# Kernel tuning notes

Hardware: AMD Instinct MI355X
Metric: run time of the kernel (lower is better)

Reference implementation:

```python
import math
import jax, jax.numpy as jnp
import numpy as np

B, W, C = 2, 2048, 1024
N, K = 16, 64  # heads, head dim (C // N)


def setup_inputs() -> dict:
    key = jax.random.key(0)
    ks = jax.random.split(key, 6)
    return {
        "in_sequence_bwc": jax.random.normal(ks[0], (B, W, C), dtype=jnp.float32),
        "W_proj": jax.random.normal(ks[1], (C, C), dtype=jnp.float32) * (1.0 / math.sqrt(C)),
        "b_proj": jax.random.normal(ks[2], (C,), dtype=jnp.float32) * 0.01,
        "generators_1nwk": jax.random.normal(ks[3], (1, N, W, K), dtype=jnp.float32),
        "W_mix": jax.random.normal(ks[4], (C, C), dtype=jnp.float32) * (1.0 / math.sqrt(C)),
        "b_mix": jax.random.normal(ks[5], (C,), dtype=jnp.float32) * 0.01,
    }


def reference(in_sequence_bwc, W_proj, b_proj, generators_1nwk, W_mix, b_mix):
    b, w, c = in_sequence_bwc.shape
    # shared projection (torch Linear: x @ W.T + b)
    p_bwc = in_sequence_bwc @ W_proj.T + b_proj
    p_bnwk = p_bwc.reshape(b, w, N, K).transpose(0, 2, 1, 3)  # [b, n, w, k]
    g_nwk = generators_1nwk[0, :, :w, :]  # [n, w, k]
    # data-dependent metric generator: p^T @ G -> [b, n, k, k]
    m_bnkk = jnp.einsum("bnwk,nwl->bnkl", p_bnwk, g_nwk)
    tril_kk = jnp.tril(jnp.ones((K, K), dtype=in_sequence_bwc.dtype))
    m_bnkk = m_bnkk * tril_kk  # lower-triangular mask on k x k
    m_bnkk = m_bnkk @ jnp.swapaxes(m_bnkk, -1, -2)  # PSD metric M M^T
    # bilinear scores: P @ M @ P^T, scaled
    pm_bnwk = jnp.einsum("bnwk,bnkl->bnwl", p_bnwk, m_bnkk)
    scores_bnww = jnp.einsum("bnwk,bnvk->bnwv", pm_bnwk, p_bnwk) / math.sqrt(K)
    causal = jnp.tril(jnp.ones((w, w), dtype=bool))
    scores_bnww = jnp.where(causal, scores_bnww, -jnp.inf)
    attn_bnww = jax.nn.softmax(scores_bnww, axis=-1)
    nudged_bnwk = attn_bnww @ p_bnwk
    nudged_bwc = nudged_bnwk.transpose(0, 2, 1, 3).reshape(b, w, c)
    return nudged_bwc @ W_mix.T + b_mix
```

## Files before the change

### kernel.cpp

```cpp
#include <hip/hip_runtime.h>
#include <math.h>

#define B_  2
#define W_  2048
#define C_  1024
#define NH_ 16
#define KD_ 64

__device__ __forceinline__ int sw(int r, int c) {
    return (r << 6) + ((((c >> 2) ^ ((r >> 2) & 7)) << 2) | (c & 3));
}

__device__ __forceinline__ void stage64s(const float* __restrict__ src,
                                         float* dst, int tid) {
#pragma unroll
    for (int q = 0; q < 4; ++q) {
        int idx = tid + (q << 8);
        int r   = idx >> 4;
        int c   = (idx & 15) << 2;
        *(float4*)&dst[sw(r, c)] = *(const float4*)(src + (idx << 2));
    }
}

__device__ __forceinline__ void stage64(const float* __restrict__ src,
                                        float (*dst)[68], int tid) {
#pragma unroll
    for (int q = 0; q < 4; ++q) {
        int idx = tid + (q << 8);
        int e   = idx << 2;
        int r   = e >> 6;
        int c   = e & 63;
        *(float4*)&dst[r][c] = *(const float4*)(src + e);
    }
}

template<int OUT_P_LAYOUT>
__global__ __launch_bounds__(256, 2)
void gemm_nt(const float* __restrict__ A, const float* __restrict__ Bw,
             const float* __restrict__ bias, float* __restrict__ Cout)
{
    __shared__ float As[16][68];
    __shared__ float Bs[16][68];
    const int tid = threadIdx.x;
    const int tx  = tid & 15, ty = tid >> 4;
    const int m0  = blockIdx.x << 6;
    const int n0  = blockIdx.y << 6;
    const int lrow = tid >> 2;
    const int lkq  = (tid & 3) << 2;
    const float* Ap = A  + (size_t)(m0 + lrow) * C_ + lkq;
    const float* Bp = Bw + (size_t)(n0 + lrow) * C_ + lkq;

    float acc[4][4] = {};
    for (int k0 = 0; k0 < C_; k0 += 16) {
        float4 av = *(const float4*)(Ap + k0);
        float4 bv = *(const float4*)(Bp + k0);
        __syncthreads();
        As[lkq+0][lrow] = av.x; As[lkq+1][lrow] = av.y;
        As[lkq+2][lrow] = av.z; As[lkq+3][lrow] = av.w;
        Bs[lkq+0][lrow] = bv.x; Bs[lkq+1][lrow] = bv.y;
        Bs[lkq+2][lrow] = bv.z; Bs[lkq+3][lrow] = bv.w;
        __syncthreads();
#pragma unroll
        for (int kk = 0; kk < 16; ++kk) {
            float4 a4 = *(const float4*)&As[kk][ty << 2];
            float4 b4 = *(const float4*)&Bs[kk][tx << 2];
            float am[4] = {a4.x, a4.y, a4.z, a4.w};
            float bm[4] = {b4.x, b4.y, b4.z, b4.w};
#pragma unroll
            for (int i = 0; i < 4; ++i)
#pragma unroll
                for (int j = 0; j < 4; ++j)
                    acc[i][j] = fmaf(am[i], bm[j], acc[i][j]);
        }
    }

    const int gc = n0 + (tx << 2);
    float4 bb = *(const float4*)&bias[gc];
#pragma unroll
    for (int i = 0; i < 4; ++i) {
        int gm = m0 + (ty << 2) + i;
        float4 o;
        o.x = acc[i][0] + bb.x;
        o.y = acc[i][1] + bb.y;
        o.z = acc[i][2] + bb.z;
        o.w = acc[i][3] + bb.w;
        if (OUT_P_LAYOUT) {
            int b = gm >> 11;
            int w = gm & 2047;
            int n = gc >> 6;
            int k = gc & 63;
            *(float4*)(Cout + (((size_t)(b * NH_ + n) * W_ + w) * KD_ + k)) = o;
        } else {
            *(float4*)(Cout + (size_t)gm * C_ + gc) = o;
        }
    }
}

__global__ __launch_bounds__(256, 2)
void metric_part(const float* __restrict__ p, const float* __restrict__ g,
                 float* __restrict__ part)
{
    __shared__ float Ps[32][68];
    __shared__ float Gs[32][68];
    const int ch  = blockIdx.x;
    const int bn  = blockIdx.y;
    const int n   = bn & (NH_ - 1);
    const int tid = threadIdx.x;
    const int tx  = tid & 15, ty = tid >> 4;
    const float* pb = p + (size_t)bn * W_ * KD_ + (size_t)(ch << 8) * KD_;
    const float* gb = g + (size_t)n  * W_ * KD_ + (size_t)(ch << 8) * KD_;

    float acc[4][4] = {};
    for (int w0 = 0; w0 < 256; w0 += 32) {
        __syncthreads();
#pragma unroll
        for (int q = 0; q < 2; ++q) {
            int idx = tid + (q << 8);
            int e   = idx << 2;
            int r   = e >> 6;
            int c   = e & 63;
            *(float4*)&Ps[r][c] = *(const float4*)(pb + (size_t)(w0 + r) * KD_ + c);
            *(float4*)&Gs[r][c] = *(const float4*)(gb + (size_t)(w0 + r) * KD_ + c);
        }
        __syncthreads();
#pragma unroll 8
        for (int w = 0; w < 32; ++w) {
            float4 a4 = *(const float4*)&Ps[w][ty << 2];
            float4 b4 = *(const float4*)&Gs[w][tx << 2];
            float am[4] = {a4.x, a4.y, a4.z, a4.w};
            float bm[4] = {b4.x, b4.y, b4.z, b4.w};
#pragma unroll
            for (int i = 0; i < 4; ++i)
#pragma unroll
                for (int j = 0; j < 4; ++j)
                    acc[i][j] = fmaf(am[i], bm[j], acc[i][j]);
        }
    }

    float* ob = part + (size_t)(bn * 8 + ch) * KD_ * KD_;
#pragma unroll
    for (int i = 0; i < 4; ++i) {
        float4 o; o.x = acc[i][0]; o.y = acc[i][1]; o.z = acc[i][2]; o.w = acc[i][3];
        *(float4*)(ob + ((ty << 2) + i) * KD_ + (tx << 2)) = o;
    }
}

__global__ __launch_bounds__(256, 2)
void metric_reduce(const float* __restrict__ part, float* __restrict__ m2)
{
    __shared__ float M1s[64][68];
    const int bn  = blockIdx.x;
    const int tid = threadIdx.x;
    const int tx  = tid & 15, ty = tid >> 4;
    const float* pb = part + (size_t)bn * 8 * KD_ * KD_;

#pragma unroll
    for (int v = 0; v < 4; ++v) {
        int f = tid + (v << 8);
        int e = f << 2;
        float4 s = *(const float4*)(pb + e);
#pragma unroll
        for (int c = 1; c < 8; ++c) {
            float4 t = *(const float4*)(pb + c * 4096 + e);
            s.x += t.x; s.y += t.y; s.z += t.z; s.w += t.w;
        }
        int k = e >> 6, l = e & 63;
        if (l + 0 > k) s.x = 0.f;
        if (l + 1 > k) s.y = 0.f;
        if (l + 2 > k) s.z = 0.f;
        if (l + 3 > k) s.w = 0.f;
        *(float4*)&M1s[k][l] = s;
    }
    __syncthreads();

    float a2[4][4] = {};
#pragma unroll
    for (int jq = 0; jq < 64; jq += 4) {
        float4 av[4], bv[4];
#pragma unroll
        for (int i = 0; i < 4; ++i) av[i] = *(const float4*)&M1s[(ty << 2) + i][jq];
#pragma unroll
        for (int j = 0; j < 4; ++j) bv[j] = *(const float4*)&M1s[(tx << 2) + j][jq];
#pragma unroll
        for (int i = 0; i < 4; ++i)
#pragma unroll
            for (int j = 0; j < 4; ++j)
                a2[i][j] += av[i].x * bv[j].x + av[i].y * bv[j].y +
                            av[i].z * bv[j].z + av[i].w * bv[j].w;
    }

    float* ob = m2 + (size_t)bn * KD_ * KD_;
#pragma unroll
    for (int i = 0; i < 4; ++i) {
        float4 o; o.x = a2[i][0]; o.y = a2[i][1]; o.z = a2[i][2]; o.w = a2[i][3];
        *(float4*)(ob + ((ty << 2) + i) * KD_ + (tx << 2)) = o;
    }
}

__global__ __launch_bounds__(256, 2)
void qgen_k(const float* __restrict__ p, const float* __restrict__ m2,
            float* __restrict__ qout)
{
    __shared__ float Pt[64][68];
    __shared__ float Ms[64][68];
    const int bn  = blockIdx.y;
    const int w0  = blockIdx.x << 6;
    const int tid = threadIdx.x;
    const int tx  = tid & 15, ty = tid >> 4;
    const float* pb = p  + (size_t)bn * W_ * KD_ + (size_t)w0 * KD_;
    const float* mb = m2 + (size_t)bn * KD_ * KD_;

    stage64(pb, Pt, tid);
    stage64(mb, Ms, tid);
    __syncthreads();

    float acc[4][4] = {};
#pragma unroll
    for (int kq = 0; kq < 64; kq += 4) {
        float4 av[4];
        float  bm[4][4];
#pragma unroll
        for (int i = 0; i < 4; ++i) av[i] = *(const float4*)&Pt[(ty << 2) + i][kq];
#pragma unroll
        for (int kk = 0; kk < 4; ++kk) {
            float4 t = *(const float4*)&Ms[kq + kk][tx << 2];
            bm[kk][0] = t.x; bm[kk][1] = t.y; bm[kk][2] = t.z; bm[kk][3] = t.w;
        }
#pragma unroll
        for (int i = 0; i < 4; ++i) {
            float am[4] = {av[i].x, av[i].y, av[i].z, av[i].w};
#pragma unroll
            for (int j = 0; j < 4; ++j)
                acc[i][j] = fmaf(am[0], bm[0][j],
                            fmaf(am[1], bm[1][j],
                            fmaf(am[2], bm[2][j],
                            fmaf(am[3], bm[3][j], acc[i][j]))));
        }
    }

    float* ob = qout + (size_t)bn * W_ * KD_ + (size_t)w0 * KD_;
#pragma unroll
    for (int i = 0; i < 4; ++i) {
        float4 o;
        o.x = acc[i][0] * 0.125f; o.y = acc[i][1] * 0.125f;
        o.z = acc[i][2] * 0.125f; o.w = acc[i][3] * 0.125f;
        *(float4*)(ob + ((ty << 2) + i) * KD_ + (tx << 2)) = o;
    }
}

__global__ __launch_bounds__(256, 2)
void attn_k(const float* __restrict__ qg, const float* __restrict__ p,
            float* __restrict__ nud)
{
    __shared__ float Qs[4096];
    __shared__ float Ks[4096];
    __shared__ float Es[4096];
    const int bid = blockIdx.x;
    const int bn  = bid & 31;
    const int qt  = 31 - (bid >> 5);
    const int b   = bn >> 4, n = bn & 15;
    const int tid = threadIdx.x;
    const int tx  = tid & 15, ty = tid >> 4;
    const float* qb = qg + (size_t)bn * W_ * KD_ + (size_t)(qt << 6) * KD_;
    const float* kb = p  + (size_t)bn * W_ * KD_;

    stage64s(qb, Qs, tid);

    float acc[4][4] = {};
    float mi[4], li[4];
#pragma unroll
    for (int i = 0; i < 4; ++i) { mi[i] = -INFINITY; li[i] = 0.f; }

    for (int j0 = 0; j0 <= qt; ++j0) {
        __syncthreads();
        stage64s(kb + (size_t)(j0 << 6) * KD_, Ks, tid);
        __syncthreads();

        float s[4][4] = {};
#pragma unroll
        for (int kq = 0; kq < 64; kq += 4) {
            float4 av[4], bv[4];
#pragma unroll
            for (int i = 0; i < 4; ++i) av[i] = *(const float4*)&Qs[sw((ty << 2) + i, kq)];
#pragma unroll
            for (int j = 0; j < 4; ++j) bv[j] = *(const float4*)&Ks[sw((tx << 2) + j, kq)];
#pragma unroll
            for (int i = 0; i < 4; ++i)
#pragma unroll
                for (int j = 0; j < 4; ++j)
                    s[i][j] = fmaf(av[i].x, bv[j].x,
                              fmaf(av[i].y, bv[j].y,
                              fmaf(av[i].z, bv[j].z,
                              fmaf(av[i].w, bv[j].w, s[i][j]))));
        }

        if (j0 == qt) {
#pragma unroll
            for (int i = 0; i < 4; ++i)
#pragma unroll
                for (int j = 0; j < 4; ++j)
                    if (((tx << 2) + j) > ((ty << 2) + i)) s[i][j] = -INFINITY;
        }

        float mnew[4], al[4];
#pragma unroll
        for (int i = 0; i < 4; ++i) {
            float rm = fmaxf(fmaxf(s[i][0], s[i][1]), fmaxf(s[i][2], s[i][3]));
            rm = fmaxf(rm, __shfl_xor(rm, 1, 16));
            rm = fmaxf(rm, __shfl_xor(rm, 2, 16));
            rm = fmaxf(rm, __shfl_xor(rm, 4, 16));
            rm = fmaxf(rm, __shfl_xor(rm, 8, 16));
            mnew[i] = fmaxf(mi[i], rm);
        }
#pragma unroll
        for (int i = 0; i < 4; ++i) {
#pragma unroll
            for (int j = 0; j < 4; ++j) s[i][j] = __expf(s[i][j] - mnew[i]);
            float rs = s[i][0] + s[i][1] + s[i][2] + s[i][3];
            rs += __shfl_xor(rs, 1, 16);
            rs += __shfl_xor(rs, 2, 16);
            rs += __shfl_xor(rs, 4, 16);
            rs += __shfl_xor(rs, 8, 16);
            al[i] = __expf(mi[i] - mnew[i]);
            li[i] = li[i] * al[i] + rs;
            mi[i] = mnew[i];
        }
#pragma unroll
        for (int i = 0; i < 4; ++i) {
            float4 e; e.x = s[i][0]; e.y = s[i][1]; e.z = s[i][2]; e.w = s[i][3];
            *(float4*)&Es[sw((ty << 2) + i, tx << 2)] = e;
#pragma unroll
            for (int j = 0; j < 4; ++j) acc[i][j] *= al[i];
        }
        __syncthreads();

#pragma unroll
        for (int jq = 0; jq < 64; jq += 4) {
            float4 av[4];
            float  vm[4][4];
#pragma unroll
            for (int i = 0; i < 4; ++i) av[i] = *(const float4*)&Es[sw((ty << 2) + i, jq)];
#pragma unroll
            for (int kk = 0; kk < 4; ++kk) {
                float4 t = *(const float4*)&Ks[sw(jq + kk, tx << 2)];
                vm[kk][0] = t.x; vm[kk][1] = t.y; vm[kk][2] = t.z; vm[kk][3] = t.w;
            }
#pragma unroll
            for (int i = 0; i < 4; ++i) {
                float am[4] = {av[i].x, av[i].y, av[i].z, av[i].w};
#pragma unroll
                for (int c = 0; c < 4; ++c)
                    acc[i][c] = fmaf(am[0], vm[0][c],
                                fmaf(am[1], vm[1][c],
                                fmaf(am[2], vm[2][c],
                                fmaf(am[3], vm[3][c], acc[i][c]))));
            }
        }
    }

    const int wrow = qt << 6;
#pragma unroll
    for (int i = 0; i < 4; ++i) {
        float inv = 1.f / li[i];
        float4 o;
        o.x = acc[i][0] * inv; o.y = acc[i][1] * inv;
        o.z = acc[i][2] * inv; o.w = acc[i][3] * inv;
        size_t row = (size_t)(b * W_ + wrow + (ty << 2) + i);
        *(float4*)(nud + row * C_ + (n << 6) + (tx << 2)) = o;
    }
}

extern "C" void kernel_launch(void* const* d_in, const int* in_sizes, int n_in,
                              void* d_out, int out_size, void* d_ws, size_t ws_size,
                              hipStream_t stream)
{
    (void)in_sizes; (void)n_in; (void)out_size; (void)ws_size;
    const float* X  = (const float*)d_in[0];
    const float* Wp = (const float*)d_in[1];
    const float* bp = (const float*)d_in[2];
    const float* G  = (const float*)d_in[3];
    const float* Wm = (const float*)d_in[4];
    const float* bm = (const float*)d_in[5];
    float* out = (float*)d_out;
    float* ws  = (float*)d_ws;

    float* Pbuf = ws;
    float* Qbuf = ws + 4194304;
    float* M2   = ws + 8388608;
    float* Nud  = ws + 8519680;
    float* Part = Qbuf;

    dim3 blk(256);
    gemm_nt<1>   <<<dim3(64, 16), blk, 0, stream>>>(X, Wp, bp, Pbuf);
    metric_part  <<<dim3(8, 32),  blk, 0, stream>>>(Pbuf, G, Part);
    metric_reduce<<<dim3(32),     blk, 0, stream>>>(Part, M2);
    qgen_k       <<<dim3(32, 32), blk, 0, stream>>>(Pbuf, M2, Qbuf);
    attn_k       <<<dim3(1024),   blk, 0, stream>>>(Qbuf, Pbuf, Nud);
    gemm_nt<0>   <<<dim3(64, 16), blk, 0, stream>>>(Nud, Wm, bm, out);
}
```

Baseline: 842.6 us.

## Use 128x128 register-prefetched GEMMs and fuse Q generation into 128-row attention

```diff
diff --git a/kernel.cpp b/kernel.cpp
--- a/kernel.cpp
+++ b/kernel.cpp
@@ -7,91 +7,104 @@
 #define NH_ 16
 #define KD_ 64
 
-__device__ __forceinline__ int sw(int r, int c) {
+__device__ __forceinline__ int swz2(int r, int c) {
     return (r << 6) + ((((c >> 2) ^ ((r >> 2) & 7)) << 2) | (c & 3));
 }
-
-__device__ __forceinline__ void stage64s(const float* __restrict__ src,
-                                         float* dst, int tid) {
-#pragma unroll
-    for (int q = 0; q < 4; ++q) {
-        int idx = tid + (q << 8);
-        int r   = idx >> 4;
-        int c   = (idx & 15) << 2;
-        *(float4*)&dst[sw(r, c)] = *(const float4*)(src + (idx << 2));
-    }
-}
-
-__device__ __forceinline__ void stage64(const float* __restrict__ src,
-                                        float (*dst)[68], int tid) {
-#pragma unroll
-    for (int q = 0; q < 4; ++q) {
-        int idx = tid + (q << 8);
-        int e   = idx << 2;
-        int r   = e >> 6;
-        int c   = e & 63;
-        *(float4*)&dst[r][c] = *(const float4*)(src + e);
+__device__ __forceinline__ int swz3(int r, int c) {
+    return (r << 6) + ((((c >> 2) ^ ((r >> 3) & 7)) << 2) | (c & 3));
+}
+
+__device__ __forceinline__ void stage_sw2(const float* __restrict__ src,
+                                          float* dst, int tid, int nf4) {
+    for (int idx = tid; idx < nf4; idx += 256) {
+        int r = idx >> 4;
+        int c = (idx & 15) << 2;
+        *(float4*)&dst[swz2(r, c)] = *(const float4*)(src + (idx << 2));
     }
 }
 
 template<int OUT_P_LAYOUT>
 __global__ __launch_bounds__(256, 2)
-void gemm_nt(const float* __restrict__ A, const float* __restrict__ Bw,
+void gemm128(const float* __restrict__ A, const float* __restrict__ Bw,
              const float* __restrict__ bias, float* __restrict__ Cout)
 {
-    __shared__ float As[16][68];
-    __shared__ float Bs[16][68];
+    __shared__ float As[8192];
+    __shared__ float Bs[8192];
     const int tid = threadIdx.x;
     const int tx  = tid & 15, ty = tid >> 4;
-    const int m0  = blockIdx.x << 6;
-    const int n0  = blockIdx.y << 6;
-    const int lrow = tid >> 2;
-    const int lkq  = (tid & 3) << 2;
-    const float* Ap = A  + (size_t)(m0 + lrow) * C_ + lkq;
-    const float* Bp = Bw + (size_t)(n0 + lrow) * C_ + lkq;
-
-    float acc[4][4] = {};
-    for (int k0 = 0; k0 < C_; k0 += 16) {
-        float4 av = *(const float4*)(Ap + k0);
-        float4 bv = *(const float4*)(Bp + k0);
-        __syncthreads();
-        As[lkq+0][lrow] = av.x; As[lkq+1][lrow] = av.y;
-        As[lkq+2][lrow] = av.z; As[lkq+3][lrow] = av.w;
-        Bs[lkq+0][lrow] = bv.x; Bs[lkq+1][lrow] = bv.y;
-        Bs[lkq+2][lrow] = bv.z; Bs[lkq+3][lrow] = bv.w;
-        __syncthreads();
-#pragma unroll
-        for (int kk = 0; kk < 16; ++kk) {
-            float4 a4 = *(const float4*)&As[kk][ty << 2];
-            float4 b4 = *(const float4*)&Bs[kk][tx << 2];
-            float am[4] = {a4.x, a4.y, a4.z, a4.w};
-            float bm[4] = {b4.x, b4.y, b4.z, b4.w};
-#pragma unroll
-            for (int i = 0; i < 4; ++i)
-#pragma unroll
-                for (int j = 0; j < 4; ++j)
-                    acc[i][j] = fmaf(am[i], bm[j], acc[i][j]);
-        }
-    }
-
-    const int gc = n0 + (tx << 2);
-    float4 bb = *(const float4*)&bias[gc];
-#pragma unroll
-    for (int i = 0; i < 4; ++i) {
-        int gm = m0 + (ty << 2) + i;
-        float4 o;
-        o.x = acc[i][0] + bb.x;
-        o.y = acc[i][1] + bb.y;
-        o.z = acc[i][2] + bb.z;
-        o.w = acc[i][3] + bb.w;
-        if (OUT_P_LAYOUT) {
-            int b = gm >> 11;
-            int w = gm & 2047;
-            int n = gc >> 6;
-            int k = gc & 63;
-            *(float4*)(Cout + (((size_t)(b * NH_ + n) * W_ + w) * KD_ + k)) = o;
-        } else {
-            *(float4*)(Cout + (size_t)gm * C_ + gc) = o;
+    const int m0  = blockIdx.x << 7;
+    const int n0  = blockIdx.y << 7;
+
+    float4 ra[8], rb[8];
+    int rr[8], cc[8];
+#pragma unroll
+    for (int t = 0; t < 8; ++t) {
+        int idx = tid + (t << 8);
+        rr[t] = idx >> 4;
+        cc[t] = (idx & 15) << 2;
+    }
+#pragma unroll
+    for (int t = 0; t < 8; ++t) {
+        ra[t] = *(const float4*)(A  + (size_t)(m0 + rr[t]) * C_ + cc[t]);
+        rb[t] = *(const float4*)(Bw + (size_t)(n0 + rr[t]) * C_ + cc[t]);
+    }
+
+    float acc[8][8] = {};
+    for (int kb = 0; kb < 16; ++kb) {
+        __syncthreads();
+#pragma unroll
+        for (int t = 0; t < 8; ++t) {
+            *(float4*)&As[swz3(rr[t], cc[t])] = ra[t];
+            *(float4*)&Bs[swz3(rr[t], cc[t])] = rb[t];
+        }
+        __syncthreads();
+        if (kb < 15) {
+            int k0 = (kb + 1) << 6;
+#pragma unroll
+            for (int t = 0; t < 8; ++t) {
+                ra[t] = *(const float4*)(A  + (size_t)(m0 + rr[t]) * C_ + k0 + cc[t]);
+                rb[t] = *(const float4*)(Bw + (size_t)(n0 + rr[t]) * C_ + k0 + cc[t]);
+            }
+        }
+#pragma unroll
+        for (int kq = 0; kq < 64; kq += 4) {
+            float4 av[8], bv[8];
+#pragma unroll
+            for (int i = 0; i < 8; ++i) av[i] = *(const float4*)&As[swz3((ty << 3) + i, kq)];
+#pragma unroll
+            for (int j = 0; j < 8; ++j) bv[j] = *(const float4*)&Bs[swz3((tx << 3) + j, kq)];
+#pragma unroll
+            for (int i = 0; i < 8; ++i)
+#pragma unroll
+                for (int j = 0; j < 8; ++j)
+                    acc[i][j] = fmaf(av[i].x, bv[j].x,
+                                fmaf(av[i].y, bv[j].y,
+                                fmaf(av[i].z, bv[j].z,
+                                fmaf(av[i].w, bv[j].w, acc[i][j]))));
+        }
+    }
+
+#pragma unroll
+    for (int h = 0; h < 2; ++h) {
+        int gc = n0 + (tx << 3) + (h << 2);
+        float4 bb = *(const float4*)&bias[gc];
+#pragma unroll
+        for (int i = 0; i < 8; ++i) {
+            int gm = m0 + (ty << 3) + i;
+            float4 o;
+            o.x = acc[i][(h << 2) + 0] + bb.x;
+            o.y = acc[i][(h << 2) + 1] + bb.y;
+            o.z = acc[i][(h << 2) + 2] + bb.z;
+            o.w = acc[i][(h << 2) + 3] + bb.w;
+            if (OUT_P_LAYOUT) {
+                int b = gm >> 11;
+                int w = gm & 2047;
+                int n = gc >> 6;
+                int k = gc & 63;
+                *(float4*)(Cout + (((size_t)(b * NH_ + n) * W_ + w) * KD_ + k)) = o;
+            } else {
+                *(float4*)(Cout + (size_t)gm * C_ + gc) = o;
+            }
         }
     }
 }
@@ -198,174 +211,143 @@
 }
 
 __global__ __launch_bounds__(256, 2)
-void qgen_k(const float* __restrict__ p, const float* __restrict__ m2,
-            float* __restrict__ qout)
-{
-    __shared__ float Pt[64][68];
-    __shared__ float Ms[64][68];
-    const int bn  = blockIdx.y;
-    const int w0  = blockIdx.x << 6;
-    const int tid = threadIdx.x;
-    const int tx  = tid & 15, ty = tid >> 4;
-    const float* pb = p  + (size_t)bn * W_ * KD_ + (size_t)w0 * KD_;
-    const float* mb = m2 + (size_t)bn * KD_ * KD_;
-
-    stage64(pb, Pt, tid);
-    stage64(mb, Ms, tid);
-    __syncthreads();
-
-    float acc[4][4] = {};
-#pragma unroll
-    for (int kq = 0; kq < 64; kq += 4) {
-        float4 av[4];
-        float  bm[4][4];
-#pragma unroll
-        for (int i = 0; i < 4; ++i) av[i] = *(const float4*)&Pt[(ty << 2) + i][kq];
-#pragma unroll
-        for (int kk = 0; kk < 4; ++kk) {
-            float4 t = *(const float4*)&Ms[kq + kk][tx << 2];
-            bm[kk][0] = t.x; bm[kk][1] = t.y; bm[kk][2] = t.z; bm[kk][3] = t.w;
-        }
-#pragma unroll
-        for (int i = 0; i < 4; ++i) {
-            float am[4] = {av[i].x, av[i].y, av[i].z, av[i].w};
-#pragma unroll
-            for (int j = 0; j < 4; ++j)
-                acc[i][j] = fmaf(am[0], bm[0][j],
-                            fmaf(am[1], bm[1][j],
-                            fmaf(am[2], bm[2][j],
-                            fmaf(am[3], bm[3][j], acc[i][j]))));
-        }
-    }
-
-    float* ob = qout + (size_t)bn * W_ * KD_ + (size_t)w0 * KD_;
-#pragma unroll
-    for (int i = 0; i < 4; ++i) {
-        float4 o;
-        o.x = acc[i][0] * 0.125f; o.y = acc[i][1] * 0.125f;
-        o.z = acc[i][2] * 0.125f; o.w = acc[i][3] * 0.125f;
-        *(float4*)(ob + ((ty << 2) + i) * KD_ + (tx << 2)) = o;
-    }
-}
-
-__global__ __launch_bounds__(256, 2)
-void attn_k(const float* __restrict__ qg, const float* __restrict__ p,
-            float* __restrict__ nud)
-{
-    __shared__ float Qs[4096];
+void attn_k2(const float* __restrict__ p, const float* __restrict__ m2,
+             float* __restrict__ nud)
+{
+    __shared__ float Qs[8192];
     __shared__ float Ks[4096];
-    __shared__ float Es[4096];
+    __shared__ float Es[8192];
     const int bid = blockIdx.x;
     const int bn  = bid & 31;
-    const int qt  = 31 - (bid >> 5);
+    const int qt  = 15 - (bid >> 5);
     const int b   = bn >> 4, n = bn & 15;
     const int tid = threadIdx.x;
     const int tx  = tid & 15, ty = tid >> 4;
-    const float* qb = qg + (size_t)bn * W_ * KD_ + (size_t)(qt << 6) * KD_;
-    const float* kb = p  + (size_t)bn * W_ * KD_;
-
-    stage64s(qb, Qs, tid);
-
-    float acc[4][4] = {};
-    float mi[4], li[4];
-#pragma unroll
-    for (int i = 0; i < 4; ++i) { mi[i] = -INFINITY; li[i] = 0.f; }
-
-    for (int j0 = 0; j0 <= qt; ++j0) {
-        __syncthreads();
-        stage64s(kb + (size_t)(j0 << 6) * KD_, Ks, tid);
-        __syncthreads();
-
-        float s[4][4] = {};
+    const float* pb = p + (size_t)bn * W_ * KD_;
+    const float* qb = pb + (size_t)(qt << 7) * KD_;
+
+    stage_sw2(qb, Es, tid, 2048);
+    stage_sw2(m2 + (size_t)bn * KD_ * KD_, Ks, tid, 1024);
+    __syncthreads();
+    {
+        float qacc[8][4] = {};
 #pragma unroll
         for (int kq = 0; kq < 64; kq += 4) {
-            float4 av[4], bv[4];
-#pragma unroll
-            for (int i = 0; i < 4; ++i) av[i] = *(const float4*)&Qs[sw((ty << 2) + i, kq)];
-#pragma unroll
-            for (int j = 0; j < 4; ++j) bv[j] = *(const float4*)&Ks[sw((tx << 2) + j, kq)];
-#pragma unroll
-            for (int i = 0; i < 4; ++i)
+            float4 av[8], bm[4];
+#pragma unroll
+            for (int i = 0; i < 8; ++i) av[i] = *(const float4*)&Es[swz2((ty << 3) + i, kq)];
+#pragma unroll
+            for (int kk = 0; kk < 4; ++kk) bm[kk] = *(const float4*)&Ks[swz2(kq + kk, tx << 2)];
+#pragma unroll
+            for (int i = 0; i < 8; ++i) {
+                qacc[i][0] = fmaf(av[i].x, bm[0].x, fmaf(av[i].y, bm[1].x,
+                             fmaf(av[i].z, bm[2].x, fmaf(av[i].w, bm[3].x, qacc[i][0]))));
+                qacc[i][1] = fmaf(av[i].x, bm[0].y, fmaf(av[i].y, bm[1].y,
+                             fmaf(av[i].z, bm[2].y, fmaf(av[i].w, bm[3].y, qacc[i][1]))));
+                qacc[i][2] = fmaf(av[i].x, bm[0].z, fmaf(av[i].y, bm[1].z,
+                             fmaf(av[i].z, bm[2].z, fmaf(av[i].w, bm[3].z, qacc[i][2]))));
+                qacc[i][3] = fmaf(av[i].x, bm[0].w, fmaf(av[i].y, bm[1].w,
+                             fmaf(av[i].z, bm[2].w, fmaf(av[i].w, bm[3].w, qacc[i][3]))));
+            }
+        }
+#pragma unroll
+        for (int i = 0; i < 8; ++i) {
+            float4 o;
+            o.x = qacc[i][0] * 0.125f; o.y = qacc[i][1] * 0.125f;
+            o.z = qacc[i][2] * 0.125f; o.w = qacc[i][3] * 0.125f;
+            *(float4*)&Qs[swz2((ty << 3) + i, tx << 2)] = o;
+        }
+    }
+
+    float acc[8][4] = {};
+    float mi[8], li[8];
+#pragma unroll
+    for (int i = 0; i < 8; ++i) { mi[i] = -INFINITY; li[i] = 0.f; }
+
+    const int j0max = (qt << 1) + 1;
+    for (int j0 = 0; j0 <= j0max; ++j0) {
+        __syncthreads();
+        stage_sw2(pb + (size_t)(j0 << 6) * KD_, Ks, tid, 1024);
+        __syncthreads();
+
+        float s[8][4] = {};
+#pragma unroll
+        for (int kq = 0; kq < 64; kq += 4) {
+            float4 bv[4];
+#pragma unroll
+            for (int j = 0; j < 4; ++j) bv[j] = *(const float4*)&Ks[swz2((tx << 2) + j, kq)];
+#pragma unroll
+            for (int i = 0; i < 8; ++i) {
+                float4 a = *(const float4*)&Qs[swz2((ty << 3) + i, kq)];
 #pragma unroll
                 for (int j = 0; j < 4; ++j)
-                    s[i][j] = fmaf(av[i].x, bv[j].x,
-                              fmaf(av[i].y, bv[j].y,
-                              fmaf(av[i].z, bv[j].z,
-                              fmaf(av[i].w, bv[j].w, s[i][j]))));
-        }
-
-        if (j0 == qt) {
-#pragma unroll
-            for (int i = 0; i < 4; ++i)
+                    s[i][j] = fmaf(a.x, bv[j].x, fmaf(a.y, bv[j].y,
+                              fmaf(a.z, bv[j].z, fmaf(a.w, bv[j].w, s[i][j]))));
+            }
+        }
+
+        if (j0 >= (qt << 1)) {
+            int cbase = (j0 << 6) - (qt << 7) + (tx << 2);
+#pragma unroll
+            for (int i = 0; i < 8; ++i)
 #pragma unroll
                 for (int j = 0; j < 4; ++j)
-                    if (((tx << 2) + j) > ((ty << 2) + i)) s[i][j] = -INFINITY;
-        }
-
-        float mnew[4], al[4];
-#pragma unroll
-        for (int i = 0; i < 4; ++i) {
+                    if (cbase + j > (ty << 3) + i) s[i][j] = -INFINITY;
+        }
+
+#pragma unroll
+        for (int i = 0; i < 8; ++i) {
             float rm = fmaxf(fmaxf(s[i][0], s[i][1]), fmaxf(s[i][2], s[i][3]));
             rm = fmaxf(rm, __shfl_xor(rm, 1, 16));
             rm = fmaxf(rm, __shfl_xor(rm, 2, 16));
             rm = fmaxf(rm, __shfl_xor(rm, 4, 16));
             rm = fmaxf(rm, __shfl_xor(rm, 8, 16));
-            mnew[i] = fmaxf(mi[i], rm);
-        }
-#pragma unroll
-        for (int i = 0; i < 4; ++i) {
-#pragma unroll
-            for (int j = 0; j < 4; ++j) s[i][j] = __expf(s[i][j] - mnew[i]);
+            float mnew = fmaxf(mi[i], rm);
+#pragma unroll
+            for (int j = 0; j < 4; ++j) s[i][j] = __expf(s[i][j] - mnew);
             float rs = s[i][0] + s[i][1] + s[i][2] + s[i][3];
             rs += __shfl_xor(rs, 1, 16);
             rs += __shfl_xor(rs, 2, 16);
             rs += __shfl_xor(rs, 4, 16);
             rs += __shfl_xor(rs, 8, 16);
-            al[i] = __expf(mi[i] - mnew[i]);
-            li[i] = li[i] * al[i] + rs;
-            mi[i] = mnew[i];
-        }
-#pragma unroll
-        for (int i = 0; i < 4; ++i) {
+            float al = __expf(mi[i] - mnew);
+            li[i] = li[i] * al + rs;
+            mi[i] = mnew;
             float4 e; e.x = s[i][0]; e.y = s[i][1]; e.z = s[i][2]; e.w = s[i][3];
-            *(float4*)&Es[sw((ty << 2) + i, tx << 2)] = e;
-#pragma unroll
-            for (int j = 0; j < 4; ++j) acc[i][j] *= al[i];
+            *(float4*)&Es[swz2((ty << 3) + i, tx << 2)] = e;
+#pragma unroll
+            for (int j = 0; j < 4; ++j) acc[i][j] *= al;
         }
         __syncthreads();
 
 #pragma unroll
         for (int jq = 0; jq < 64; jq += 4) {
-            float4 av[4];
-            float  vm[4][4];
-#pragma unroll
-            for (int i = 0; i < 4; ++i) av[i] = *(const float4*)&Es[sw((ty << 2) + i, jq)];
-#pragma unroll
-            for (int kk = 0; kk < 4; ++kk) {
-                float4 t = *(const float4*)&Ks[sw(jq + kk, tx << 2)];
-                vm[kk][0] = t.x; vm[kk][1] = t.y; vm[kk][2] = t.z; vm[kk][3] = t.w;
-            }
-#pragma unroll
-            for (int i = 0; i < 4; ++i) {
-                float am[4] = {av[i].x, av[i].y, av[i].z, av[i].w};
-#pragma unroll
-                for (int c = 0; c < 4; ++c)
-                    acc[i][c] = fmaf(am[0], vm[0][c],
-                                fmaf(am[1], vm[1][c],
-                                fmaf(am[2], vm[2][c],
-                                fmaf(am[3], vm[3][c], acc[i][c]))));
-            }
-        }
-    }
-
-    const int wrow = qt << 6;
-#pragma unroll
-    for (int i = 0; i < 4; ++i) {
+            float4 vm[4];
+#pragma unroll
+            for (int kk = 0; kk < 4; ++kk) vm[kk] = *(const float4*)&Ks[swz2(jq + kk, tx << 2)];
+#pragma unroll
+            for (int i = 0; i < 8; ++i) {
+                float4 a = *(const float4*)&Es[swz2((ty << 3) + i, jq)];
+                acc[i][0] = fmaf(a.x, vm[0].x, fmaf(a.y, vm[1].x,
+                            fmaf(a.z, vm[2].x, fmaf(a.w, vm[3].x, acc[i][0]))));
+                acc[i][1] = fmaf(a.x, vm[0].y, fmaf(a.y, vm[1].y,
+                            fmaf(a.z, vm[2].y, fmaf(a.w, vm[3].y, acc[i][1]))));
+                acc[i][2] = fmaf(a.x, vm[0].z, fmaf(a.y, vm[1].z,
+                            fmaf(a.z, vm[2].z, fmaf(a.w, vm[3].z, acc[i][2]))));
+                acc[i][3] = fmaf(a.x, vm[0].w, fmaf(a.y, vm[1].w,
+                            fmaf(a.z, vm[2].w, fmaf(a.w, vm[3].w, acc[i][3]))));
+            }
+        }
+    }
+
+    const int wrow = qt << 7;
+#pragma unroll
+    for (int i = 0; i < 8; ++i) {
         float inv = 1.f / li[i];
         float4 o;
         o.x = acc[i][0] * inv; o.y = acc[i][1] * inv;
         o.z = acc[i][2] * inv; o.w = acc[i][3] * inv;
-        size_t row = (size_t)(b * W_ + wrow + (ty << 2) + i);
+        size_t row = (size_t)(b * W_ + wrow + (ty << 3) + i);
         *(float4*)(nud + row * C_ + (n << 6) + (tx << 2)) = o;
     }
 }
@@ -385,16 +367,14 @@
     float* ws  = (float*)d_ws;
 
     float* Pbuf = ws;
-    float* Qbuf = ws + 4194304;
+    float* Part = ws + 4194304;
     float* M2   = ws + 8388608;
     float* Nud  = ws + 8519680;
-    float* Part = Qbuf;
 
     dim3 blk(256);
-    gemm_nt<1>   <<<dim3(64, 16), blk, 0, stream>>>(X, Wp, bp, Pbuf);
-    metric_part  <<<dim3(8, 32),  blk, 0, stream>>>(Pbuf, G, Part);
-    metric_reduce<<<dim3(32),     blk, 0, stream>>>(Part, M2);
-    qgen_k       <<<dim3(32, 32), blk, 0, stream>>>(Pbuf, M2, Qbuf);
-    attn_k       <<<dim3(1024),   blk, 0, stream>>>(Qbuf, Pbuf, Nud);
-    gemm_nt<0>   <<<dim3(64, 16), blk, 0, stream>>>(Nud, Wm, bm, out);
-}
+    gemm128<1>   <<<dim3(32, 8), blk, 0, stream>>>(X, Wp, bp, Pbuf);
+    metric_part  <<<dim3(8, 32), blk, 0, stream>>>(Pbuf, G, Part);
+    metric_reduce<<<dim3(32),    blk, 0, stream>>>(Part, M2);
+    attn_k2      <<<dim3(512),   blk, 0, stream>>>(Pbuf, M2, Nud);
+    gemm128<0>   <<<dim3(32, 8), blk, 0, stream>>>(Nud, Wm, bm, out);
+}
```

Result: slower. 1.511 ms (+79.4%).
